# Kernel optimization log

Measured on AMD Instinct MI355X. Metric: run time of the kernel, lower is better.

## Reference

```python
import jax, jax.numpy as jnp
import numpy as np

B, S, D = 32, 256, 384
N_LAYERS, N_HEAD, D_HEAD, D_INNER, K = 6, 1, 64, 1536, 3
DP_FILT, N_MEL, N_EMBED, PAD_IDX = 256, 80, 41, 0
PACE, MEL_MAX, MAX_DUR = 0.0265, 400, 75.0
ATTN_SCALE = 1.0 / float(np.sqrt(D_HEAD))


def layer_norm(x, g, b, eps=1e-5):
    mu = x.mean(-1, keepdims=True)
    v = ((x - mu) ** 2).mean(-1, keepdims=True)
    return (x - mu) * jax.lax.rsqrt(v + eps) * g + b


def conv1d(x, w, b, pad):
    # x: [B,T,Cin], w: [Cout,Cin,K] (torch layout) -> [B,T,Cout]
    y = jax.lax.conv_general_dilated(x, jnp.transpose(w, (2, 1, 0)), (1,), [(pad, pad)],
                                     dimension_numbers=('NWC', 'WIO', 'NWC'))
    return y + b


def pos_embedding(T, d):
    inv = 1.0 / (10000.0 ** (jnp.arange(0, d, 2, dtype=jnp.float32) / d))
    s = jnp.arange(T, dtype=jnp.float32)[:, None] * inv[None, :]
    return jnp.concatenate([jnp.sin(s), jnp.cos(s)], axis=-1)  # [T,d]


def fft_stack(x, mask, params):
    # x: [B,T,D], mask: [B,T,1]; params: tuple of arrays stacked over layers
    key_ok = (mask[..., 0] > 0)[:, None, None, :]  # [B,1,1,T]

    def body(h, p):
        qkv_w, qkv_b, o_w, ln1g, ln1b, c1w, c1b, c2w, c2b, ln2g, ln2b = p
        Bv, T, _ = h.shape
        qkv = h @ qkv_w + qkv_b
        q, k, v = [t.reshape(Bv, T, N_HEAD, D_HEAD) for t in jnp.split(qkv, 3, axis=-1)]
        sc = jnp.einsum('bqhd,bkhd->bhqk', q, k) * ATTN_SCALE
        a = jax.nn.softmax(jnp.where(key_ok, sc, -1e9), axis=-1)
        vec = jnp.einsum('bhqk,bkhd->bqhd', a, v).reshape(Bv, T, N_HEAD * D_HEAD)
        h = layer_norm(h + vec @ o_w, ln1g, ln1b) * mask   # post-norm MHA, then TransformerLayer mask
        c = jax.nn.relu(conv1d(h, c1w, c1b, (K - 1) // 2))
        c = conv1d(c, c2w, c2b, (K - 1) // 2)
        h = layer_norm(h + c, ln2g, ln2b) * mask           # post-norm conv-FF
        return h, None

    h, _ = jax.lax.scan(body, x, params)
    return h


def reference(inputs, dur_tgt, emb,
              enc_qkv_w, enc_qkv_b, enc_o_w, enc_ln1_g, enc_ln1_b,
              enc_c1_w, enc_c1_b, enc_c2_w, enc_c2_b, enc_ln2_g, enc_ln2_b,
              dec_qkv_w, dec_qkv_b, dec_o_w, dec_ln1_g, dec_ln1_b,
              dec_c1_w, dec_c1_b, dec_c2_w, dec_c2_b, dec_ln2_g, dec_ln2_b,
              dp_c1_w, dp_c1_b, dp_ln1_g, dp_ln1_b, dp_c2_w, dp_c2_b, dp_ln2_g, dp_ln2_b,
              dp_fc_w, dp_fc_b, proj_w, proj_b):
    # ---- encoder FFT (embed_input=True) ----
    enc_mask = (inputs != PAD_IDX)[..., None].astype(jnp.float32)  # [B,S,1]
    x = emb[inputs] + pos_embedding(S, D)[None] * enc_mask
    enc_out = fft_stack(x, enc_mask, (enc_qkv_w, enc_qkv_b, enc_o_w, enc_ln1_g, enc_ln1_b,
                                      enc_c1_w, enc_c1_b, enc_c2_w, enc_c2_b, enc_ln2_g, enc_ln2_b))
    h = enc_out * enc_mask
    h = layer_norm(jax.nn.relu(conv1d(h, dp_c1_w, dp_c1_b, K // 2)), dp_ln1_g, dp_ln1_b)
    h = layer_norm(jax.nn.relu(conv1d(h, dp_c2_w, dp_c2_b, K // 2)), dp_ln2_g, dp_ln2_b)
    log_dur_pred = ((h @ dp_fc_w + dp_fc_b) * enc_mask)[..., 0]
    dur_pred = jnp.clip(jnp.exp(log_dur_pred) - 1.0, 0.0, MAX_DUR)
    # ---- regulate_len (pace hardcoded to 0.0265; use_gt_durations=True path) ----
    reps = jnp.round(jax.lax.stop_gradient(dur_tgt) / PACE).astype(jnp.int32)  # .long() in torch
    cum = jnp.cumsum(reps, axis=1)          # [B,S]
    total = cum[:, -1]                      # full (unclipped) decoder lengths
    pos = jnp.arange(MEL_MAX)
    # frame t of sample b comes from phoneme i with cum[i-1] <= t < cum[i]
    idx = jax.vmap(lambda c: jnp.searchsorted(c, pos, side='right'))(cum)  # [B,MEL_MAX]
    idx = jnp.clip(idx, 0, S - 1)
    enc_rep = jax.vmap(lambda e, i: e[i])(enc_out, idx)  # [B,MEL_MAX,D]
    dec_lens = jnp.minimum(total, MEL_MAX)
    dec_mask = (pos[None, :] < dec_lens[:, None])[..., None].astype(jnp.float32)
    enc_rep = jnp.where(dec_mask > 0, enc_rep, 40.0)  # pad_sequence padding_value=40.0
    # ---- decoder FFT (embed_input=False) ----
    y = enc_rep + pos_embedding(MEL_MAX, D)[None] * dec_mask
    dec_out = fft_stack(y, dec_mask, (dec_qkv_w, dec_qkv_b, dec_o_w, dec_ln1_g, dec_ln1_b,
                                      dec_c1_w, dec_c1_b, dec_c2_w, dec_c2_b, dec_ln2_g, dec_ln2_b))
    mel_out = dec_out @ proj_w + proj_b
    return (mel_out, dec_mask, dur_pred, log_dur_pred, dec_lens)


def setup_inputs() -> dict:
    key = jax.random.key(0)
    ks = jax.random.split(key, 16)
    w = lambda k, shape: jax.random.normal(k, shape, dtype=jnp.float32) * 0.02
    L, A = N_LAYERS, 3 * N_HEAD * D_HEAD
    inputs = jax.random.randint(ks[0], (B, S), 0, N_EMBED, dtype=jnp.int32)
    # durations ~ U(0, 0.06) seconds -> repeats in {0,1,2}, ragged total lengths around MEL_MAX
    dur_tgt = jax.random.uniform(ks[1], (B, S), dtype=jnp.float32) * 0.06
    emb = w(ks[2], (N_EMBED, D)).at[PAD_IDX].set(0.0)
    d = dict(inputs=inputs, dur_tgt=dur_tgt, emb=emb)
    for name, k0 in (('enc', 3), ('dec', 7)):
        d[name + '_qkv_w'] = w(ks[k0], (L, D, A)); d[name + '_qkv_b'] = jnp.zeros((L, A))
        d[name + '_o_w'] = w(ks[k0 + 1], (L, N_HEAD * D_HEAD, D))
        d[name + '_ln1_g'] = jnp.ones((L, D)); d[name + '_ln1_b'] = jnp.zeros((L, D))
        d[name + '_c1_w'] = w(ks[k0 + 2], (L, D_INNER, D, K)); d[name + '_c1_b'] = jnp.zeros((L, D_INNER))
        d[name + '_c2_w'] = w(ks[k0 + 3], (L, D, D_INNER, K)); d[name + '_c2_b'] = jnp.zeros((L, D))
        d[name + '_ln2_g'] = jnp.ones((L, D)); d[name + '_ln2_b'] = jnp.zeros((L, D))
    d['dp_c1_w'] = w(ks[11], (DP_FILT, D, K)); d['dp_c1_b'] = jnp.zeros((DP_FILT,))
    d['dp_ln1_g'] = jnp.ones((DP_FILT,)); d['dp_ln1_b'] = jnp.zeros((DP_FILT,))
    d['dp_c2_w'] = w(ks[12], (DP_FILT, DP_FILT, K)); d['dp_c2_b'] = jnp.zeros((DP_FILT,))
    d['dp_ln2_g'] = jnp.ones((DP_FILT,)); d['dp_ln2_b'] = jnp.zeros((DP_FILT,))
    d['dp_fc_w'] = w(ks[13], (DP_FILT, 1)); d['dp_fc_b'] = jnp.zeros((1,))
    d['proj_w'] = w(ks[14], (D, N_MEL)); d['proj_b'] = jnp.zeros((N_MEL,))
    return d
```

## Files before the change

### kernel.cpp

```cpp
#include <hip/hip_runtime.h>
#include <hip/hip_bf16.h>
#include <stdint.h>

typedef __attribute__((ext_vector_type(8))) short bf16x8;
typedef __attribute__((ext_vector_type(4))) float f32x4;
typedef __attribute__((ext_vector_type(4))) unsigned int u32x4;

static constexpr int BB = 32, SS = 256, DD = 384;
static constexpr int TDEC = 400;
static constexpr int NMELC = 80;

static constexpr size_t OFF_MEL    = 0;
static constexpr size_t OFF_DMASK  = (size_t)BB * TDEC * NMELC;
static constexpr size_t OFF_DUR    = OFF_DMASK + (size_t)BB * TDEC;
static constexpr size_t OFF_LOGDUR = OFF_DUR + (size_t)BB * SS;
static constexpr size_t OFF_DLEN   = OFF_LOGDUR + (size_t)BB * SS;

__device__ __forceinline__ void gld16(void* lds, const void* g) {
  __builtin_amdgcn_global_load_lds(
      (const __attribute__((address_space(1))) void*)g,
      (__attribute__((address_space(3))) void*)lds, 16, 0, 0);
}


__global__ __launch_bounds__(256)
void transpose_cvt(const float* __restrict__ src, __hip_bfloat16* __restrict__ dst,
                   int R, int C, int Cpad)
{
  __shared__ float tile[32][33];
  int l = blockIdx.z;
  src += (size_t)l * R * C;
  dst += (size_t)l * Cpad * R;
  int r0 = blockIdx.x * 32, c0 = blockIdx.y * 32;
  int tx = threadIdx.x, ty = threadIdx.y;
  for (int i = ty; i < 32; i += 8) {
    int c = c0 + tx;
    tile[i][tx] = (c < C) ? src[(size_t)(r0 + i) * C + c] : 0.f;
  }
  __syncthreads();
  for (int i = ty; i < 32; i += 8) {
    dst[(size_t)(c0 + i) * R + (r0 + tx)] = __float2bfloat16(tile[tx][i]);
  }
}

__global__ __launch_bounds__(256)
void conv_cvt(const float* __restrict__ src, __hip_bfloat16* __restrict__ dst,
              int Cout, int Cin, long long total)
{
  long long i = (long long)blockIdx.x * 256 + threadIdx.x;
  if (i >= total) return;
  int ci = (int)(i % Cin);
  long long t1 = i / Cin;
  int co = (int)(t1 % Cout);
  long long t2 = t1 / Cout;
  int tap = (int)(t2 % 3);
  int l = (int)(t2 / 3);
  dst[i] = __float2bfloat16(src[(((size_t)l * Cout + co) * Cin + ci) * 3 + tap]);
}


__global__ __launch_bounds__(256)
void pe_kernel(float* __restrict__ pe, int T)
{
  int i = blockIdx.x * 256 + threadIdx.x;
  if (i >= T * 192) return;
  int t = i / 192, j = i % 192;
  float inv = expf(-(float)j * (9.210340371976184f / 192.f));
  float s = (float)t * inv;
  pe[(size_t)t * 384 + j]       = sinf(s);
  pe[(size_t)t * 384 + 192 + j] = cosf(s);
}

__global__ __launch_bounds__(128)
void embed_kernel(const int* __restrict__ inputs, const float* __restrict__ emb,
                  const float* __restrict__ pe, float* __restrict__ maskf,
                  __hip_bfloat16* __restrict__ xb)
{
  int blk = blockIdx.x; int b = blk / SS, t = blk % SS;
  int tok = inputs[b * SS + t];
  float mk = (tok != 0) ? 1.f : 0.f;
  if (threadIdx.x == 0) maskf[b * SS + t] = mk;
  size_t prow = ((size_t)b * (SS + 2) + 1 + t) * 384;
  for (int c = threadIdx.x; c < 384; c += 128) {
    float v = emb[(size_t)tok * 384 + c] + pe[(size_t)t * 384 + c] * mk;
    xb[prow + c] = __float2bfloat16(v);
  }
}

__global__ __launch_bounds__(256)
void zero_guards(__hip_bfloat16* __restrict__ buf, int T, int C)
{
  int b = blockIdx.x >> 1, which = blockIdx.x & 1;
  size_t row = ((size_t)b * (T + 2) + (which ? (T + 1) : 0)) * (size_t)C;
  for (int c = threadIdx.x; c < C; c += 256) buf[row + c] = __float2bfloat16(0.f);
}

template<int TM, int TN, int DEPTH, int NTAPS, int KV, bool DUAL,
         bool RELU, bool OUTF32, bool CPAD>
__global__ __launch_bounds__(256)
void gemm_tn(const __hip_bfloat16* __restrict__ A,
             const __hip_bfloat16* __restrict__ Bw,
             const float* __restrict__ bias,
             void* __restrict__ Cout_,
             int N, int ldc, int T, int Npad)
{
  constexpr int KS = KV >> 5;
  constexpr int NSTEP = NTAPS * KS;
  constexpr int NI = DUAL ? NSTEP / 2 : NSTEP;
  constexpr int DEP = (DEPTH < NI) ? DEPTH : NI;
  constexpr int NBUF = DEP + 1;
  constexpr int ABYTES = TM * 64;
  constexpr int BBYTES = TN * 64;
  constexpr int HALF = ABYTES + BBYTES;
  constexpr int BUFB = DUAL ? 2 * HALF : HALF;
  constexpr int MI_N = TM / 32;
  constexpr int NI_N = TN / 32;
  constexpr int OPS1 = (TM == 128 ? 2 : 1) + (TN == 128 ? 2 : 1);
  constexpr int OPS = DUAL ? 2 * OPS1 : OPS1;
  __shared__ __align__(16) char SH[NBUF * BUFB];

  const int tid = threadIdx.x;
  const int lane = tid & 63;
  const int w = tid >> 6;
  const int wm = w >> 1, wn = w & 1;

  const int GN = gridDim.y;
  const int NB = gridDim.x * GN;
  const int f = blockIdx.y * gridDim.x + blockIdx.x;
  const int qq = NB >> 3, rr8 = NB & 7;
  const int xcd = f & 7, pos = f >> 3;
  const int st = (xcd < rr8) ? xcd * (qq + 1) : rr8 * (qq + 1) + (xcd - rr8) * qq;
  const int L = st + pos;
  const int m0 = (L / GN) * TM;
  const int n0 = (L % GN) * TN;

  const int ar = tid >> 2;
  const int q = tid & 3;
  const int qsw = q ^ ((ar >> 1) & 3);
  const int g0 = m0 + ar, g1 = g0 + 64;
  const char* sA0 = (const char*)A + (((size_t)(g0 + 2 * (g0 / T) + 1 - NTAPS / 2)) * KV + qsw * 8) * 2;
  const char* sA1 = (const char*)A + (((size_t)(g1 + 2 * (g1 / T) + 1 - NTAPS / 2)) * KV + qsw * 8) * 2;
  const char* sB0 = (const char*)Bw + ((size_t)(n0 + ar) * KV + qsw * 8) * 2;
  const char* sB1 = (const char*)Bw + ((size_t)(n0 + ar + 64) * KV + qsw * 8) * 2;

  const int woff = ar * 64 + q * 16;
  int tap_s = 0;

  const size_t AROW = (size_t)KV * 2;
  const size_t BPAN = (size_t)Npad * KV * 2;

  auto ADV = [&]() {
    sA0 += AROW; sA1 += AROW; sB0 += BPAN; sB1 += BPAN;
    if (++tap_s == NTAPS) {
      tap_s = 0;
      sA0 -= NTAPS * AROW - 64; sA1 -= NTAPS * AROW - 64;
      sB0 -= NTAPS * BPAN - 64; sB1 -= NTAPS * BPAN - 64;
    }
  };
  auto STAGE1 = [&](char* base) {
    gld16(base + woff, sA0);
    if (TM == 128) gld16(base + 4096 + woff, sA1);
    gld16(base + ABYTES + woff, sB0);
    if (TN == 128) gld16(base + ABYTES + 4096 + woff, sB1);
    ADV();
  };
  auto STAGE = [&](int buf) {
    char* base = SH + buf * BUFB;
    STAGE1(base);
    if (DUAL) STAGE1(base + HALF);
  };

  f32x4 zero = {0.f, 0.f, 0.f, 0.f};
  f32x4 acc[MI_N][NI_N];
#pragma unroll
  for (int i = 0; i < MI_N; i++)
#pragma unroll
    for (int j = 0; j < NI_N; j++) acc[i][j] = zero;

  const int rl = lane & 15;
  const int hi4 = lane >> 4;
  const int kb2 = (hi4 ^ ((rl >> 1) & 3)) * 16;

  auto COMPUTE = [&](const char* base) {
    const char* Ab = base;
    const char* Bb = base + ABYTES;
    bf16x8 af[MI_N], bfr[NI_N];
#pragma unroll
    for (int mi = 0; mi < MI_N; mi++)
      af[mi] = *(const bf16x8*)(Ab + (wm * (TM / 2) + mi * 16 + rl) * 64 + kb2);
#pragma unroll
    for (int ni = 0; ni < NI_N; ni++)
      bfr[ni] = *(const bf16x8*)(Bb + (wn * (TN / 2) + ni * 16 + rl) * 64 + kb2);
#pragma unroll
    for (int mi = 0; mi < MI_N; mi++)
#pragma unroll
      for (int ni = 0; ni < NI_N; ni++)
        acc[mi][ni] = __builtin_amdgcn_mfma_f32_16x16x32_bf16(af[mi], bfr[ni], acc[mi][ni], 0, 0, 0);
  };

#pragma unroll
  for (int i = 0; i < DEP; ++i) STAGE(i);
  if constexpr (DEP == NI) {
    asm volatile("s_waitcnt vmcnt(0)" ::: "memory");
  } else {
    asm volatile("s_waitcnt vmcnt(%0)" :: "i"((DEP - 1) * OPS) : "memory");
  }
  __builtin_amdgcn_s_barrier();
  __builtin_amdgcn_sched_barrier(0);

  int cur = 0;
  for (int i = 0; i < NI; ++i) {
    if (i + DEP < NI) {
      int nb = cur + DEP; if (nb >= NBUF) nb -= NBUF;
      STAGE(nb);
    }
    const char* base = SH + cur * BUFB;
    COMPUTE(base);
    if (DUAL) COMPUTE(base + HALF);
    if (i + 1 < NI) {
      if (i + DEP < NI) {
        asm volatile("s_waitcnt vmcnt(%0)" :: "i"((DEP - 1) * OPS) : "memory");
      } else {
        asm volatile("s_waitcnt vmcnt(0)" ::: "memory");
      }
      __builtin_amdgcn_s_barrier();
      __builtin_amdgcn_sched_barrier(0);
    }
    cur = cur + 1; if (cur >= NBUF) cur -= NBUF;
  }

  const int rj = hi4 * 4;
  if (!OUTF32) {
    __syncthreads();
    ushort* S = (ushort*)SH;
#pragma unroll
    for (int mi = 0; mi < MI_N; mi++) {
#pragma unroll
      for (int ni = 0; ni < NI_N; ni++) {
        int lc = wn * (TN / 2) + ni * 16 + rl;
        float bv = bias ? bias[n0 + lc] : 0.f;
#pragma unroll
        for (int j = 0; j < 4; j++) {
          float v = acc[mi][ni][j] + bv;
          if (RELU) v = fmaxf(v, 0.f);
          __hip_bfloat16 hb = __float2bfloat16(v);
          S[(wm * (TM / 2) + mi * 16 + rj + j) * TN + lc] = *(ushort*)&hb;
        }
      }
    }
    __syncthreads();
    constexpr int TPR = TN / 8;
    constexpr int RPP = 256 / TPR;
    const int tr = tid / TPR;
    const int tc = (tid % TPR) * 8;
#pragma unroll
    for (int pass = 0; pass < TM / RPP; ++pass) {
      int lr = pass * RPP + tr;
      int gcol = n0 + tc;
      if (gcol < N) {
        int r = m0 + lr;
        size_t orow = CPAD ? ((size_t)r + 2 * (r / T) + 1) : (size_t)r;
        *(u32x4*)((__hip_bfloat16*)Cout_ + orow * ldc + gcol) = *(const u32x4*)&S[lr * TN + tc];
      }
    }
  } else {
#pragma unroll
    for (int mi = 0; mi < MI_N; mi++) {
#pragma unroll
      for (int ni = 0; ni < NI_N; ni++) {
        int col = n0 + wn * (TN / 2) + ni * 16 + rl;
        if (col < N) {
          float bv = bias ? bias[col] : 0.f;
#pragma unroll
          for (int j = 0; j < 4; j++) {
            int r = m0 + wm * (TM / 2) + mi * 16 + rj + j;
            float v = acc[mi][ni][j] + bv;
            if (RELU) v = fmaxf(v, 0.f);
            size_t orow = CPAD ? ((size_t)r + 2 * (r / T) + 1) : (size_t)r;
            ((float*)Cout_)[orow * ldc + col] = v;
          }
        }
      }
    }
  }
}

__global__ __launch_bounds__(256)
void fattn_kernel(const __hip_bfloat16* __restrict__ qkv, const float* __restrict__ maskf,
                  __hip_bfloat16* __restrict__ vec, int T, int NT)
{
  __shared__ __align__(16) ushort VT[64][456];
  __shared__ __align__(16) ushort Pl[4][16][72];
  __shared__ float MS[448];

  const int tid = threadIdx.x;
  const int b = blockIdx.y;
  const int TP = T + 2;
  const int KTOT = NT * 64;
  const char* bptr = (const char*)qkv + ((size_t)b * TP + 1) * 384;

  for (int k = tid; k < KTOT; k += 256)
    MS[k] = (k < T) ? ((maskf[b * T + k] > 0.f) ? 0.f : -1e9f) : -1e38f;
  for (int i = tid; i < KTOT * 8; i += 256) {
    int k = i >> 3, seg = i & 7;
    int kr = (k < T) ? k : T - 1;
    uint4 u = *(const uint4*)(bptr + (size_t)kr * 384 + 256 + seg * 16);
    const ushort* e = (const ushort*)&u;
#pragma unroll
    for (int j = 0; j < 8; ++j) VT[seg * 8 + j][k] = e[j];
  }
  __syncthreads();

  const int w = tid >> 6, lane = tid & 63;
  const int lo = lane & 15, hi = lane >> 4;
  const int q0 = blockIdx.x * 64 + w * 16;
  const int qc = min(q0 + lo, T - 1);

  bf16x8 afr[2];
#pragma unroll
  for (int ks = 0; ks < 2; ++ks)
    afr[ks] = *(const bf16x8*)(bptr + (size_t)qc * 384 + ks * 64 + hi * 16);

  f32x4 Oacc[4];
  f32x4 z = {0.f, 0.f, 0.f, 0.f};
#pragma unroll
  for (int df = 0; df < 4; ++df) Oacc[df] = z;
  float mrun[4], lrun[4];
#pragma unroll
  for (int j = 0; j < 4; ++j) { mrun[j] = -3e38f; lrun[j] = 0.f; }

  for (int kt = 0; kt < NT; ++kt) {
    const int kb = kt * 64;
    f32x4 S[4];
#pragma unroll
    for (int f = 0; f < 4; ++f) S[f] = z;
#pragma unroll
    for (int ks = 0; ks < 2; ++ks) {
#pragma unroll
      for (int f = 0; f < 4; ++f) {
        int krc = min(kb + f * 16 + lo, T - 1);
        bf16x8 bfr = *(const bf16x8*)(bptr + (size_t)krc * 384 + 128 + ks * 64 + hi * 16);
        S[f] = __builtin_amdgcn_mfma_f32_16x16x32_bf16(afr[ks], bfr, S[f], 0, 0, 0);
      }
    }
    float sv[4][4];
#pragma unroll
    for (int f = 0; f < 4; ++f) {
      float msel = MS[kb + f * 16 + lo];
#pragma unroll
      for (int j = 0; j < 4; ++j) {
        float x = S[f][j] * 0.125f;
        sv[f][j] = (msel == 0.f) ? x : msel;
      }
    }
    float scale[4];
#pragma unroll
    for (int j = 0; j < 4; ++j) {
      float m4 = fmaxf(fmaxf(sv[0][j], sv[1][j]), fmaxf(sv[2][j], sv[3][j]));
#pragma unroll
      for (int msk = 1; msk < 16; msk <<= 1) m4 = fmaxf(m4, __shfl_xor(m4, msk));
      float mnew = fmaxf(mrun[j], m4);
      scale[j] = __expf(mrun[j] - mnew);
      mrun[j] = mnew;
    }
    float pv[4][4], ps[4] = {0.f, 0.f, 0.f, 0.f};
#pragma unroll
    for (int f = 0; f < 4; ++f)
#pragma unroll
      for (int j = 0; j < 4; ++j) {
        float p = __expf(sv[f][j] - mrun[j]);
        pv[f][j] = p; ps[j] += p;
      }
#pragma unroll
    for (int j = 0; j < 4; ++j) {
#pragma unroll
      for (int msk = 1; msk < 16; msk <<= 1) ps[j] += __shfl_xor(ps[j], msk);
      lrun[j] = lrun[j] * scale[j] + ps[j];
#pragma unroll
      for (int df = 0; df < 4; ++df) Oacc[df][j] *= scale[j];
    }
#pragma unroll
    for (int f = 0; f < 4; ++f)
#pragma unroll
      for (int j = 0; j < 4; ++j) {
        __hip_bfloat16 hb = __float2bfloat16(pv[f][j]);
        Pl[w][hi * 4 + j][f * 16 + lo] = *(ushort*)&hb;
      }
#pragma unroll
    for (int ks = 0; ks < 2; ++ks) {
      bf16x8 pa = *(const bf16x8*)((const char*)&Pl[w][lo][0] + ks * 64 + hi * 16);
#pragma unroll
      for (int df = 0; df < 4; ++df) {
        bf16x8 vfr = *(const bf16x8*)((const char*)&VT[df * 16 + lo][0] + kb * 2 + ks * 64 + hi * 16);
        Oacc[df] = __builtin_amdgcn_mfma_f32_16x16x32_bf16(pa, vfr, Oacc[df], 0, 0, 0);
      }
    }
  }

  float inv[4];
#pragma unroll
  for (int j = 0; j < 4; ++j) inv[j] = 1.f / lrun[j];
#pragma unroll
  for (int df = 0; df < 4; ++df)
#pragma unroll
    for (int j = 0; j < 4; ++j) {
      int qq = q0 + hi * 4 + j;
      if (qq < T) {
        __hip_bfloat16 hb = __float2bfloat16(Oacc[df][j] * inv[j]);
        *(ushort*)((char*)vec + ((size_t)b * TP + 1 + qq) * 128 + (df * 16 + lo) * 2) = *(ushort*)&hb;
      }
    }
}

template<int C, bool HASRES, bool HASMASK>
__global__ __launch_bounds__(256)
void ln_kernel(const __hip_bfloat16* __restrict__ xin, const __hip_bfloat16* __restrict__ resin,
               const float* __restrict__ g, const float* __restrict__ bb,
               const float* __restrict__ maskf,
               __hip_bfloat16* __restrict__ outb, int T)
{
  constexpr int NU = C / 128;
  const int row = blockIdx.x * 4 + (threadIdx.x >> 6);
  const int lane = threadIdx.x & 63;
  const int b = row / T, t = row - b * T;
  const size_t prow = ((size_t)b * (T + 2) + 1 + t) * C;
  const uint* xu = (const uint*)(xin + prow);
  const uint* ru = (const uint*)(resin + prow);
  float v[2 * NU];
  float s1 = 0.f, s2 = 0.f;
#pragma unroll
  for (int k = 0; k < NU; ++k) {
    uint ux = xu[lane + 64 * k];
    uint xl = ux << 16, xh = ux & 0xffff0000u;
    float lo = *(float*)&xl, hi = *(float*)&xh;
    if (HASRES) {
      uint ur = ru[lane + 64 * k];
      uint rl2 = ur << 16, rh = ur & 0xffff0000u;
      lo += *(float*)&rl2; hi += *(float*)&rh;
    }
    v[2 * k] = lo; v[2 * k + 1] = hi;
    s1 += lo + hi; s2 += lo * lo + hi * hi;
  }
#pragma unroll
  for (int o = 32; o > 0; o >>= 1) { s1 += __shfl_xor(s1, o); s2 += __shfl_xor(s2, o); }
  float mu = s1 / C;
  float var = s2 / C - mu * mu;
  float rstd = rsqrtf(fmaxf(var, 0.f) + 1e-5f);
  float mk = HASMASK ? maskf[row] : 1.f;
  uint* ou = (uint*)(outb + prow);
#pragma unroll
  for (int k = 0; k < NU; ++k) {
    int c = (lane + 64 * k) * 2;
    float2 gv = *(const float2*)(g + c);
    float2 bv = *(const float2*)(bb + c);
    float lo = ((v[2 * k]     - mu) * rstd * gv.x + bv.x) * mk;
    float hi = ((v[2 * k + 1] - mu) * rstd * gv.y + bv.y) * mk;
    __hip_bfloat16 hl = __float2bfloat16(lo), hh = __float2bfloat16(hi);
    ou[lane + 64 * k] = (uint)(*(ushort*)&hl) | ((uint)(*(ushort*)&hh) << 16);
  }
}

__global__ __launch_bounds__(64)
void dpfc_kernel(const __hip_bfloat16* __restrict__ dp2, const float* __restrict__ fcw,
                 const float* __restrict__ fcb, const float* __restrict__ maskf,
                 float* __restrict__ logdur, float* __restrict__ durpred)
{
  int blk = blockIdx.x; int b = blk / SS, t = blk % SS;
  size_t prow = ((size_t)b * (SS + 2) + 1 + t) * 256;
  int lane = threadIdx.x;
  float a = 0.f;
  for (int c = lane; c < 256; c += 64) a += __bfloat162float(dp2[prow + c]) * fcw[c];
  for (int o = 32; o > 0; o >>= 1) a += __shfl_down(a, o);
  if (lane == 0) {
    float ld = (a + fcb[0]) * maskf[b * SS + t];
    logdur[b * SS + t] = ld;
    durpred[b * SS + t] = fminf(fmaxf(expf(ld) - 1.f, 0.f), 75.f);
  }
}

__global__ __launch_bounds__(512)
void regulator_kernel(const float* __restrict__ dur, float* __restrict__ dmaskf,
                      int* __restrict__ idxbuf, float* __restrict__ out_dmask,
                      float* __restrict__ out_dlen)
{
  int b = blockIdx.x, tid = threadIdx.x;
  __shared__ int cum[256];
  __shared__ int len_s;
  if (tid < 256) cum[tid] = (int)rintf(dur[b * 256 + tid] / 0.0265f);
  __syncthreads();
  if (tid == 0) {
    int acc = 0;
    for (int i = 0; i < 256; i++) { acc += cum[i]; cum[i] = acc; }
    int len = acc < 400 ? acc : 400;
    len_s = len;
    out_dlen[b] = (float)len;
  }
  __syncthreads();
  if (tid < 400) {
    int p = tid;
    int lo = 0, hi = 256;
    while (lo < hi) { int mid = (lo + hi) >> 1; if (cum[mid] <= p) lo = mid + 1; else hi = mid; }
    int idx = lo < 255 ? lo : 255;
    idxbuf[b * 400 + p] = idx;
    float mk = (p < len_s) ? 1.f : 0.f;
    dmaskf[b * 400 + p] = mk;
    out_dmask[b * 400 + p] = mk;
  }
}

__global__ __launch_bounds__(128)
void build_y_kernel(const __hip_bfloat16* __restrict__ encb, const int* __restrict__ idxbuf,
                    const float* __restrict__ dmaskf, const float* __restrict__ pe,
                    __hip_bfloat16* __restrict__ yb)
{
  int blk = blockIdx.x; int b = blk / 400, p = blk % 400;
  float mk = dmaskf[b * 400 + p];
  int idx = idxbuf[b * 400 + p];
  size_t orowp = ((size_t)b * 402 + 1 + p) * 384;
  size_t srow = ((size_t)b * 258 + 1 + idx) * 384;
  for (int c = threadIdx.x; c < 384; c += 128) {
    float v = (mk > 0.f) ? (__bfloat162float(encb[srow + c]) + pe[(size_t)p * 384 + c]) : 40.f;
    yb[orowp + c] = __float2bfloat16(v);
  }
}

extern "C" void kernel_launch(void* const* d_in, const int* in_sizes, int n_in,
                              void* d_out, int out_size, void* d_ws, size_t ws_size,
                              hipStream_t stream)
{
  (void)in_sizes; (void)n_in; (void)out_size; (void)ws_size;
  float* outF = (float*)d_out;

  const int*   inputs  = (const int*)d_in[0];
  const float* dur_tgt = (const float*)d_in[1];
  const float* emb     = (const float*)d_in[2];
  const float* e_qkv_w = (const float*)d_in[3];
  const float* e_qkv_b = (const float*)d_in[4];
  const float* e_o_w   = (const float*)d_in[5];
  const float* e_ln1g  = (const float*)d_in[6];
  const float* e_ln1b  = (const float*)d_in[7];
  const float* e_c1w   = (const float*)d_in[8];
  const float* e_c1b   = (const float*)d_in[9];
  const float* e_c2w   = (const float*)d_in[10];
  const float* e_c2b   = (const float*)d_in[11];
  const float* e_ln2g  = (const float*)d_in[12];
  const float* e_ln2b  = (const float*)d_in[13];
  const float* dc_qkv_w = (const float*)d_in[14];
  const float* dc_qkv_b = (const float*)d_in[15];
  const float* dc_o_w   = (const float*)d_in[16];
  const float* dc_ln1g  = (const float*)d_in[17];
  const float* dc_ln1b  = (const float*)d_in[18];
  const float* dc_c1w   = (const float*)d_in[19];
  const float* dc_c1b   = (const float*)d_in[20];
  const float* dc_c2w   = (const float*)d_in[21];
  const float* dc_c2b   = (const float*)d_in[22];
  const float* dc_ln2g  = (const float*)d_in[23];
  const float* dc_ln2b  = (const float*)d_in[24];
  const float* dp_c1w = (const float*)d_in[25];
  const float* dp_c1b = (const float*)d_in[26];
  const float* dp_ln1g = (const float*)d_in[27];
  const float* dp_ln1b = (const float*)d_in[28];
  const float* dp_c2w = (const float*)d_in[29];
  const float* dp_c2b = (const float*)d_in[30];
  const float* dp_ln2g = (const float*)d_in[31];
  const float* dp_ln2b = (const float*)d_in[32];
  const float* dp_fcw = (const float*)d_in[33];
  const float* dp_fcb = (const float*)d_in[34];
  const float* proj_w = (const float*)d_in[35];
  const float* proj_b = (const float*)d_in[36];

  char* ws = (char*)d_ws;
  size_t off = 0;
  auto alloc = [&](size_t bytes) -> char* {
    char* p = ws + off;
    off += (bytes + 255) & ~(size_t)255;
    return p;
  };

  __hip_bfloat16* qkvwt_e = (__hip_bfloat16*)alloc((size_t)6 * 256 * 384 * 2);
  __hip_bfloat16* qkvwt_d = (__hip_bfloat16*)alloc((size_t)6 * 256 * 384 * 2);
  __hip_bfloat16* owt_e   = (__hip_bfloat16*)alloc((size_t)6 * 384 * 64 * 2);
  __hip_bfloat16* owt_d   = (__hip_bfloat16*)alloc((size_t)6 * 384 * 64 * 2);
  __hip_bfloat16* c1wt_e  = (__hip_bfloat16*)alloc((size_t)6 * 3 * 1536 * 384 * 2);
  __hip_bfloat16* c1wt_d  = (__hip_bfloat16*)alloc((size_t)6 * 3 * 1536 * 384 * 2);
  __hip_bfloat16* c2wt_e  = (__hip_bfloat16*)alloc((size_t)6 * 3 * 384 * 1536 * 2);
  __hip_bfloat16* c2wt_d  = (__hip_bfloat16*)alloc((size_t)6 * 3 * 384 * 1536 * 2);
  __hip_bfloat16* dpc1wt  = (__hip_bfloat16*)alloc((size_t)3 * 256 * 384 * 2);
  __hip_bfloat16* dpc2wt  = (__hip_bfloat16*)alloc((size_t)3 * 256 * 256 * 2);
  __hip_bfloat16* projwt  = (__hip_bfloat16*)alloc((size_t)128 * 384 * 2);
  float* pe_e   = (float*)alloc((size_t)256 * 384 * 4);
  float* pe_d   = (float*)alloc((size_t)400 * 384 * 4);
  float* maskf_e = (float*)alloc((size_t)32 * 256 * 4);
  float* maskf_d = (float*)alloc((size_t)32 * 400 * 4);
  int*   idxbuf  = (int*)alloc((size_t)32 * 400 * 4);
  __hip_bfloat16* h_enc_bf = (__hip_bfloat16*)alloc((size_t)32 * 258 * 384 * 2);
  __hip_bfloat16* h_dec_bf = (__hip_bfloat16*)alloc((size_t)32 * 402 * 384 * 2);
  __hip_bfloat16* qkvbuf = (__hip_bfloat16*)alloc((size_t)32 * 402 * 192 * 2);
  __hip_bfloat16* vecbuf = (__hip_bfloat16*)alloc((size_t)32 * 402 * 64 * 2);
  __hip_bfloat16* tmp384 = (__hip_bfloat16*)alloc((size_t)32 * 402 * 384 * 2);
  __hip_bfloat16* cbuf   = (__hip_bfloat16*)alloc((size_t)32 * 402 * 1536 * 2);
  __hip_bfloat16* dp1b   = (__hip_bfloat16*)alloc((size_t)32 * 258 * 256 * 2);
  __hip_bfloat16* dp2b   = (__hip_bfloat16*)alloc((size_t)32 * 258 * 256 * 2);

  transpose_cvt<<<dim3(12, 8, 6), dim3(32, 8), 0, stream>>>(e_qkv_w, qkvwt_e, 384, 192, 256);
  transpose_cvt<<<dim3(12, 8, 6), dim3(32, 8), 0, stream>>>(dc_qkv_w, qkvwt_d, 384, 192, 256);
  transpose_cvt<<<dim3(2, 12, 6), dim3(32, 8), 0, stream>>>(e_o_w, owt_e, 64, 384, 384);
  transpose_cvt<<<dim3(2, 12, 6), dim3(32, 8), 0, stream>>>(dc_o_w, owt_d, 64, 384, 384);
  transpose_cvt<<<dim3(12, 4, 1), dim3(32, 8), 0, stream>>>(proj_w, projwt, 384, 80, 128);
  {
    long long tot = 6LL * 3 * 1536 * 384;
    int blocks = (int)((tot + 255) / 256);
    conv_cvt<<<blocks, 256, 0, stream>>>(e_c1w, c1wt_e, 1536, 384, tot);
    conv_cvt<<<blocks, 256, 0, stream>>>(dc_c1w, c1wt_d, 1536, 384, tot);
    conv_cvt<<<blocks, 256, 0, stream>>>(e_c2w, c2wt_e, 384, 1536, tot);
    conv_cvt<<<blocks, 256, 0, stream>>>(dc_c2w, c2wt_d, 384, 1536, tot);
  }
  { long long tot = 3LL * 256 * 384; conv_cvt<<<(int)((tot + 255) / 256), 256, 0, stream>>>(dp_c1w, dpc1wt, 256, 384, tot); }
  { long long tot = 3LL * 256 * 256; conv_cvt<<<(int)((tot + 255) / 256), 256, 0, stream>>>(dp_c2w, dpc2wt, 256, 256, tot); }

  pe_kernel<<<(256 * 192 + 255) / 256, 256, 0, stream>>>(pe_e, 256);
  pe_kernel<<<(400 * 192 + 255) / 256, 256, 0, stream>>>(pe_d, 400);

  embed_kernel<<<32 * 256, 128, 0, stream>>>(inputs, emb, pe_e, maskf_e, h_enc_bf);
  zero_guards<<<64, 256, 0, stream>>>(h_enc_bf, 256, 384);
  zero_guards<<<64, 256, 0, stream>>>(cbuf, 256, 1536);

  for (int l = 0; l < 6; ++l) {
    gemm_tn<64, 128, 2, 1, 384, false, false, false, true><<<dim3(128, 2), 256, 0, stream>>>(
        h_enc_bf, qkvwt_e + (size_t)l * 256 * 384, e_qkv_b + l * 192, qkvbuf,
        192, 192, 256, 256);
    fattn_kernel<<<dim3(4, 32), 256, 0, stream>>>(qkvbuf, maskf_e, vecbuf, 256, 4);
    gemm_tn<64, 128, 2, 1, 64, false, false, false, true><<<dim3(128, 3), 256, 0, stream>>>(
        vecbuf, owt_e + (size_t)l * 384 * 64, nullptr, tmp384,
        384, 384, 256, 384);
    ln_kernel<384, true, true><<<2048, 256, 0, stream>>>(
        tmp384, h_enc_bf, e_ln1g + l * 384, e_ln1b + l * 384, maskf_e, h_enc_bf, 256);
    gemm_tn<128, 128, 2, 3, 384, false, true, false, true><<<dim3(64, 12), 256, 0, stream>>>(
        h_enc_bf, c1wt_e + (size_t)l * 3 * 1536 * 384, e_c1b + l * 1536, cbuf,
        1536, 1536, 256, 1536);
    gemm_tn<64, 128, 2, 3, 1536, true, false, false, true><<<dim3(128, 3), 256, 0, stream>>>(
        cbuf, c2wt_e + (size_t)l * 3 * 384 * 1536, e_c2b + l * 384, tmp384,
        384, 384, 256, 384);
    ln_kernel<384, true, true><<<2048, 256, 0, stream>>>(
        tmp384, h_enc_bf, e_ln2g + l * 384, e_ln2b + l * 384, maskf_e, h_enc_bf, 256);
  }

  zero_guards<<<64, 256, 0, stream>>>(dp1b, 256, 256);
  gemm_tn<64, 128, 2, 3, 384, false, true, false, true><<<dim3(128, 2), 256, 0, stream>>>(
      h_enc_bf, dpc1wt, dp_c1b, dp1b, 256, 256, 256, 256);
  ln_kernel<256, false, false><<<2048, 256, 0, stream>>>(
      dp1b, nullptr, dp_ln1g, dp_ln1b, nullptr, dp1b, 256);
  gemm_tn<64, 128, 2, 3, 256, false, true, false, true><<<dim3(128, 2), 256, 0, stream>>>(
      dp1b, dpc2wt, dp_c2b, dp2b, 256, 256, 256, 256);
  ln_kernel<256, false, false><<<2048, 256, 0, stream>>>(
      dp2b, nullptr, dp_ln2g, dp_ln2b, nullptr, dp2b, 256);
  dpfc_kernel<<<32 * 256, 64, 0, stream>>>(
      dp2b, dp_fcw, dp_fcb, maskf_e, outF + OFF_LOGDUR, outF + OFF_DUR);

  regulator_kernel<<<32, 512, 0, stream>>>(dur_tgt, maskf_d, idxbuf,
                                           outF + OFF_DMASK, outF + OFF_DLEN);
  zero_guards<<<64, 256, 0, stream>>>(h_dec_bf, 400, 384);
  zero_guards<<<64, 256, 0, stream>>>(cbuf, 400, 1536);
  build_y_kernel<<<32 * 400, 128, 0, stream>>>(h_enc_bf, idxbuf, maskf_d, pe_d, h_dec_bf);

  for (int l = 0; l < 6; ++l) {
    gemm_tn<64, 128, 2, 1, 384, false, false, false, true><<<dim3(200, 2), 256, 0, stream>>>(
        h_dec_bf, qkvwt_d + (size_t)l * 256 * 384, dc_qkv_b + l * 192, qkvbuf,
        192, 192, 400, 256);
    fattn_kernel<<<dim3(7, 32), 256, 0, stream>>>(qkvbuf, maskf_d, vecbuf, 400, 7);
    gemm_tn<64, 128, 2, 1, 64, false, false, false, true><<<dim3(200, 3), 256, 0, stream>>>(
        vecbuf, owt_d + (size_t)l * 384 * 64, nullptr, tmp384,
        384, 384, 400, 384);
    ln_kernel<384, true, true><<<3200, 256, 0, stream>>>(
        tmp384, h_dec_bf, dc_ln1g + l * 384, dc_ln1b + l * 384, maskf_d, h_dec_bf, 400);
    gemm_tn<128, 128, 2, 3, 384, false, true, false, true><<<dim3(100, 12), 256, 0, stream>>>(
        h_dec_bf, c1wt_d + (size_t)l * 3 * 1536 * 384, dc_c1b + l * 1536, cbuf,
        1536, 1536, 400, 1536);
    gemm_tn<64, 128, 2, 3, 1536, true, false, false, true><<<dim3(200, 3), 256, 0, stream>>>(
        cbuf, c2wt_d + (size_t)l * 3 * 384 * 1536, dc_c2b + l * 384, tmp384,
        384, 384, 400, 384);
    ln_kernel<384, true, true><<<3200, 256, 0, stream>>>(
        tmp384, h_dec_bf, dc_ln2g + l * 384, dc_ln2b + l * 384, maskf_d, h_dec_bf, 400);
  }

  gemm_tn<64, 128, 2, 1, 384, false, false, true, false><<<dim3(200, 1), 256, 0, stream>>>(
      h_dec_bf, projwt, proj_b, outF + OFF_MEL, 80, 80, 400, 128);
}
```

Before: 2.121 ms.

## Add intra-block split-K GEMM for conv2 with per-wave K chunks and LDS reduction

Adds a new gemm_ws kernel for the second conv of the FFN (K=3*1536). Each of four waves handles its own quarter of the K chunks on a 64x64 output tile, double-buffered with direct-to-LDS loads. The partial results are then reduced through shared memory, and bias is applied before writing bf16. The goal is more blocks (64-wide N tiles instead of 128), better occupancy and less tail imbalance on the long-K GEMM. The cost is an LDS reduction epilogue and more redundant A loads across N tiles.

```diff
diff --git a/kernel.cpp b/kernel.cpp
--- a/kernel.cpp
+++ b/kernel.cpp
@@ -93,6 +93,135 @@
   int b = blockIdx.x >> 1, which = blockIdx.x & 1;
   size_t row = ((size_t)b * (T + 2) + (which ? (T + 1) : 0)) * (size_t)C;
   for (int c = threadIdx.x; c < C; c += 256) buf[row + c] = __float2bfloat16(0.f);
+}
+
+template<int NTAPS, int KV, bool RELU>
+__global__ __launch_bounds__(256)
+void gemm_ws(const __hip_bfloat16* __restrict__ A,
+             const __hip_bfloat16* __restrict__ Bw,
+             const float* __restrict__ bias,
+             __hip_bfloat16* __restrict__ Cout_,
+             int N, int ldc, int T, int Npad)
+{
+  constexpr int NSTEP = NTAPS * (KV >> 5);
+  static_assert(NSTEP % 4 == 0, "K chunks must split by 4 waves");
+  constexpr int NC = NSTEP / 4;
+  __shared__ __align__(16) char SH[65536];
+
+  const int tid = threadIdx.x;
+  const int lane = tid & 63;
+  const int w = tid >> 6;
+
+  const int GN = gridDim.y;
+  const int NB = gridDim.x * GN;
+  const int f = blockIdx.y * gridDim.x + blockIdx.x;
+  const int qq = NB >> 3, rr8 = NB & 7;
+  const int xcd = f & 7, pos = f >> 3;
+  const int st = (xcd < rr8) ? xcd * (qq + 1) : rr8 * (qq + 1) + (xcd - rr8) * qq;
+  const int L = st + pos;
+  const int m0 = (L / GN) * 64;
+  const int n0 = (L % GN) * 64;
+
+  const int l4 = lane >> 2, q = lane & 3;
+  const int qsw = q ^ ((l4 >> 1) & 3);
+  const char* baseA[4];
+  const char* baseB[4];
+#pragma unroll
+  for (int r = 0; r < 4; ++r) {
+    int grow = m0 + r * 16 + l4;
+    baseA[r] = (const char*)A + (((size_t)(grow + 2 * (grow / T) + 1 - NTAPS / 2)) * KV + qsw * 8) * 2;
+    int nrow = n0 + r * 16 + l4;
+    baseB[r] = (const char*)Bw + ((size_t)nrow * KV + qsw * 8) * 2;
+  }
+  const size_t AROW = (size_t)KV * 2;
+  const size_t BPAN = (size_t)Npad * KV * 2;
+
+  char* myb = SH + w * 16384;
+  const int lds_l = lane * 16;
+
+  auto STAGE = [&](int buf, int cidx) {
+    int tap = cidx % NTAPS, ks = cidx / NTAPS;
+    size_t aoff = (size_t)tap * AROW + (size_t)ks * 64;
+    size_t boff = (size_t)tap * BPAN + (size_t)ks * 64;
+    char* d = myb + buf * 8192;
+#pragma unroll
+    for (int r = 0; r < 4; ++r) gld16(d + r * 1024 + lds_l, baseA[r] + aoff);
+#pragma unroll
+    for (int r = 0; r < 4; ++r) gld16(d + 4096 + r * 1024 + lds_l, baseB[r] + boff);
+  };
+
+  f32x4 zero = {0.f, 0.f, 0.f, 0.f};
+  f32x4 acc[4][4];
+#pragma unroll
+  for (int i = 0; i < 4; i++)
+#pragma unroll
+    for (int j = 0; j < 4; j++) acc[i][j] = zero;
+
+  const int rl = lane & 15;
+  const int hi4 = lane >> 4;
+  const int kb2 = (hi4 ^ ((rl >> 1) & 3)) * 16;
+  const int rj = hi4 * 4;
+
+  auto COMPUTE = [&](int buf) {
+    const char* Ab = myb + buf * 8192;
+    const char* Bb = Ab + 4096;
+    bf16x8 af[4], bfr[4];
+#pragma unroll
+    for (int mi = 0; mi < 4; mi++)
+      af[mi] = *(const bf16x8*)(Ab + (mi * 16 + rl) * 64 + kb2);
+#pragma unroll
+    for (int ni = 0; ni < 4; ni++)
+      bfr[ni] = *(const bf16x8*)(Bb + (ni * 16 + rl) * 64 + kb2);
+#pragma unroll
+    for (int mi = 0; mi < 4; mi++)
+#pragma unroll
+      for (int ni = 0; ni < 4; ni++)
+        acc[mi][ni] = __builtin_amdgcn_mfma_f32_16x16x32_bf16(af[mi], bfr[ni], acc[mi][ni], 0, 0, 0);
+  };
+
+  int cidx = w;
+  STAGE(0, cidx); cidx += 4;
+  if (NC > 1) { STAGE(1, cidx); cidx += 4; }
+  for (int c = 0; c < NC; ++c) {
+    if (c + 1 < NC) asm volatile("s_waitcnt vmcnt(8)" ::: "memory");
+    else            asm volatile("s_waitcnt vmcnt(0)" ::: "memory");
+    __builtin_amdgcn_sched_barrier(0);
+    COMPUTE(c & 1);
+    if (c + 2 < NC) { STAGE(c & 1, cidx); cidx += 4; }
+  }
+
+  __syncthreads();
+  float* P = (float*)SH;
+#pragma unroll
+  for (int mi = 0; mi < 4; ++mi)
+#pragma unroll
+    for (int ni = 0; ni < 4; ++ni)
+#pragma unroll
+      for (int j = 0; j < 4; ++j)
+        P[w * 4096 + (mi * 16 + rj + j) * 64 + ni * 16 + rl] = acc[mi][ni][j];
+  __syncthreads();
+#pragma unroll
+  for (int p = 0; p < 4; ++p) {
+    int idx = p * 1024 + tid * 4;
+    f32x4 s = *(const f32x4*)(P + idx);
+    s += *(const f32x4*)(P + 4096 + idx);
+    s += *(const f32x4*)(P + 8192 + idx);
+    s += *(const f32x4*)(P + 12288 + idx);
+    int row = idx >> 6, col = idx & 63;
+    f32x4 bv = *(const f32x4*)(bias + n0 + col);
+    s += bv;
+    ushort4 h;
+#pragma unroll
+    for (int e = 0; e < 4; ++e) {
+      float v = s[e];
+      if (RELU) v = fmaxf(v, 0.f);
+      __hip_bfloat16 hb = __float2bfloat16(v);
+      ((ushort*)&h)[e] = *(ushort*)&hb;
+    }
+    int m = m0 + row;
+    size_t orow = (size_t)m + 2 * (m / T) + 1;
+    *(ushort4*)(Cout_ + orow * ldc + n0 + col) = h;
+  }
 }
 
 template<int TM, int TN, int DEPTH, int NTAPS, int KV, bool DUAL,
@@ -638,7 +767,7 @@
     gemm_tn<128, 128, 2, 3, 384, false, true, false, true><<<dim3(64, 12), 256, 0, stream>>>(
         h_enc_bf, c1wt_e + (size_t)l * 3 * 1536 * 384, e_c1b + l * 1536, cbuf,
         1536, 1536, 256, 1536);
-    gemm_tn<64, 128, 2, 3, 1536, true, false, false, true><<<dim3(128, 3), 256, 0, stream>>>(
+    gemm_ws<3, 1536, false><<<dim3(128, 6), 256, 0, stream>>>(
         cbuf, c2wt_e + (size_t)l * 3 * 384 * 1536, e_c2b + l * 384, tmp384,
         384, 384, 256, 384);
     ln_kernel<384, true, true><<<2048, 256, 0, stream>>>(
@@ -676,7 +805,7 @@
     gemm_tn<128, 128, 2, 3, 384, false, true, false, true><<<dim3(100, 12), 256, 0, stream>>>(
         h_dec_bf, c1wt_d + (size_t)l * 3 * 1536 * 384, dc_c1b + l * 1536, cbuf,
         1536, 1536, 400, 1536);
-    gemm_tn<64, 128, 2, 3, 1536, true, false, false, true><<<dim3(200, 3), 256, 0, stream>>>(
+    gemm_ws<3, 1536, false><<<dim3(200, 6), 256, 0, stream>>>(
         cbuf, c2wt_d + (size_t)l * 3 * 384 * 1536, dc_c2b + l * 384, tmp384,
         384, 384, 400, 384);
     ln_kernel<384, true, true><<<3200, 256, 0, stream>>>(
```

After: 2.062 ms (median of 3 runs). 1.03x faster.
